# Kernel optimization log

Hardware: AMD Instinct MI355X
Metric: run time of the kernel (lower is better)

The kernel has to match this reference:

```python
import jax, jax.numpy as jnp
import numpy as np

H = 64       # hidden size hard-coded in the module
NH = 4       # n_heads
S = 500      # stock_num
D = 10       # num_day
T = 40       # num_text (news per day)
FP = 3       # price features
FT = 512     # text embedding dim


def gru_scan(x, Wih, Whh, bih, bhh):
    """Single-sequence GRU (torch gate convention). x: (T, F) -> hidden states (T, H)."""
    gi = x @ Wih + bih  # (T, 3H) precompute input gates outside the scan

    def step(h, g):
        gh = h @ Whh + bhh
        r = jax.nn.sigmoid(g[:H] + gh[:H])
        z = jax.nn.sigmoid(g[H:2 * H] + gh[H:2 * H])
        n = jnp.tanh(g[2 * H:] + r * gh[2 * H:])
        h_new = (1.0 - z) * n + z * h
        return h_new, h_new

    h0 = jnp.zeros((H,), x.dtype)
    _, hs = jax.lax.scan(step, h0, gi)
    return hs


def attn_pool(hs, W, v):
    """Additive attention pooling over time. hs: (T, H) -> (H,)."""
    scores = jnp.tanh(hs @ W) @ v          # (T,)
    alpha = jax.nn.softmax(scores)
    return alpha @ hs


def _gru_params(key, fin, scale=0.08):
    k1, k2, k3, k4 = jax.random.split(key, 4)
    return (jax.random.normal(k1, (S, fin, 3 * H)) * scale,
            jax.random.normal(k2, (S, H, 3 * H)) * scale,
            jax.random.normal(k3, (S, 3 * H)) * scale,
            jax.random.normal(k4, (S, 3 * H)) * scale)


def _attn_params(key, scale=0.08):
    k1, k2 = jax.random.split(key)
    return (jax.random.normal(k1, (S, H, H)) * scale,
            jax.random.normal(k2, (S, H)) * scale)


def setup_inputs() -> dict:
    key = jax.random.key(0)
    ks = jax.random.split(key, 20)
    inp = {}
    inp['text_input'] = jax.random.normal(ks[0], (S, D, T, FT), dtype=jnp.float32)
    inp['price_input'] = jax.random.normal(ks[1], (S, D, FP), dtype=jnp.float32)
    inp['label'] = jax.random.randint(ks[2], (S,), 0, 2)
    inp['adj'] = jnp.ones((S, S), dtype=jnp.float32)
    inp['train'] = 0
    # per-stock stacked parameters
    (inp['Wih_p'], inp['Whh_p'], inp['bih_p'], inp['bhh_p']) = _gru_params(ks[3], FP)
    (inp['Wa_p'], inp['va_p']) = _attn_params(ks[4])
    (inp['Wih_t'], inp['Whh_t'], inp['bih_t'], inp['bhh_t']) = _gru_params(ks[5], FT)
    (inp['Wa_t'], inp['va_t']) = _attn_params(ks[6])
    (inp['Wih_s'], inp['Whh_s'], inp['bih_s'], inp['bhh_s']) = _gru_params(ks[7], H)
    (inp['Wa_s'], inp['va_s']) = _attn_params(ks[8])
    inp['Wb'] = jax.random.normal(ks[9], (S, H, H, H)) * 0.05   # Bilinear weight (out,in1,in2)
    inp['bb'] = jax.random.normal(ks[10], (S, H)) * 0.05
    inp['Wbl'] = jax.random.normal(ks[11], (S, H, 2)) * 0.08
    inp['bbl'] = jax.random.normal(ks[12], (S, 2)) * 0.08
    # shared cross-stock self-attention projections and final fc
    inp['Wq'] = jax.random.normal(ks[13], (H, H)) * 0.08
    inp['bq'] = jax.random.normal(ks[14], (H,)) * 0.08
    inp['Wk'] = jax.random.normal(ks[15], (H, H)) * 0.08
    inp['bk'] = jax.random.normal(ks[16], (H,)) * 0.08
    inp['Wf'] = jax.random.normal(ks[17], (H, 2)) * 0.08
    inp['bf'] = jax.random.normal(ks[18], (2,)) * 0.08
    return inp


def _forward(text_input, price_input, label,
             Wih_p, Whh_p, bih_p, bhh_p, Wa_p, va_p,
             Wih_t, Whh_t, bih_t, bhh_t, Wa_t, va_t,
             Wih_s, Whh_s, bih_s, bhh_s, Wa_s, va_s,
             Wb, bb, Wbl, bbl, Wq, bq, Wk, bk, Wf, bf):
    # ---- per-stock price encoder: GRU over days + attention pooling ----
    def enc_price(x, a, b, c, d, W, v):
        return attn_pool(gru_scan(x, a, b, c, d), W, v)
    x_price = jax.vmap(enc_price)(price_input, Wih_p, Whh_p, bih_p, bhh_p, Wa_p, va_p)  # (S, H)

    # ---- per-stock, per-day text encoder ----
    def enc_text_stock(xdays, a, b, c, d, W, v):
        return jax.vmap(lambda x: attn_pool(gru_scan(x, a, b, c, d), W, v))(xdays)  # (D, H)
    news = jax.vmap(enc_text_stock)(text_input, Wih_t, Whh_t, bih_t, bhh_t, Wa_t, va_t)  # (S, D, H)

    # ---- per-stock sequence encoder over days ----
    text_vec = jax.vmap(enc_price)(news, Wih_s, Whh_s, bih_s, bhh_s, Wa_s, va_s)  # (S, H)

    # ---- bilinear fusion: tanh(Bilinear(text, price)) ----
    combined = jnp.tanh(jnp.einsum('si,skij,sj->sk', text_vec, Wb, x_price) + bb)  # (S, H)

    # ---- per-stock blending head ----
    out_1 = jnp.tanh(jnp.einsum('si,sik->sk', combined, Wbl) + bbl)  # (S, 2)

    # ---- cross-stock multi-head self-attention (q,k projected, v identity) ----
    dh = H // NH
    q = (combined @ Wq + bq).reshape(S, NH, dh)
    k = (combined @ Wk + bk).reshape(S, NH, dh)
    v = combined.reshape(S, NH, dh)
    scores = jnp.einsum('shd,thd->hst', q, k) / (dh ** 0.5)
    attn = jax.nn.softmax(scores, axis=-1)
    attn_out = jnp.einsum('hst,thd->shd', attn, v).reshape(S, H)

    x = jax.nn.elu(attn_out @ Wf + bf)  # (S, 2)
    output = jax.nn.softmax(x + out_1, axis=1)
    # faithful to the original: CrossEntropyLoss applied to already-softmaxed output
    logp = jax.nn.log_softmax(output, axis=1)
    loss = -jnp.mean(logp[jnp.arange(S), label])
    return loss, output


def reference(text_input, price_input, label, adj, train,
              Wih_p, Whh_p, bih_p, bhh_p, Wa_p, va_p,
              Wih_t, Whh_t, bih_t, bhh_t, Wa_t, va_t,
              Wih_s, Whh_s, bih_s, bhh_s, Wa_s, va_s,
              Wb, bb, Wbl, bbl, Wq, bq, Wk, bk, Wf, bf):
    return _forward(text_input, price_input, label,
                    Wih_p, Whh_p, bih_p, bhh_p, Wa_p, va_p,
                    Wih_t, Whh_t, bih_t, bhh_t, Wa_t, va_t,
                    Wih_s, Whh_s, bih_s, bhh_s, Wa_s, va_s,
                    Wb, bb, Wbl, bbl, Wq, bq, Wk, bk, Wf, bf)
```

## Files before the change

kernel.cpp:

```cpp
#include <hip/hip_runtime.h>

#define Sn 500
#define Dn 10
#define Tn 40
#define FPn 3
#define FTn 512
#define Hn 64
#define G3 192
#define NHn 4

typedef __attribute__((ext_vector_type(8))) short bf8_t;
typedef __attribute__((ext_vector_type(4))) float f4_t;

__device__ __forceinline__ unsigned short f2bf(float f) {
    union { float f; unsigned int u; } v; v.f = f;
    unsigned int r = v.u + 0x7fffu + ((v.u >> 16) & 1u);
    return (unsigned short)(r >> 16);
}
__device__ __forceinline__ float bflo(unsigned int u) {
    union { unsigned int u; float f; } v; v.u = u << 16; return v.f;
}
__device__ __forceinline__ float bfhi(unsigned int u) {
    union { unsigned int u; float f; } v; v.u = u & 0xffff0000u; return v.f;
}
__device__ __forceinline__ unsigned int cvtpk(float lo, float hi) {
    unsigned int r;
    asm("v_cvt_pk_bf16_f32 %0, %1, %2" : "=v"(r) : "v"(lo), "v"(hi));
    return r;
}
__device__ __forceinline__ float sigmoidf_(float x) { return 1.f / (1.f + __expf(-x)); }
__device__ __forceinline__ float tanhf_(float x) {
    x = fminf(15.f, fmaxf(-15.f, x));
    float e = __expf(2.f * x);
    return (e - 1.f) / (e + 1.f);
}
__device__ __forceinline__ float dot8(uint4 wv, f4_t hA, f4_t hB) {
    return bflo(wv.x) * hA[0] + bfhi(wv.x) * hA[1]
         + bflo(wv.y) * hA[2] + bfhi(wv.y) * hA[3]
         + bflo(wv.z) * hB[0] + bfhi(wv.z) * hB[1]
         + bflo(wv.w) * hB[2] + bfhi(wv.w) * hB[3];
}
union bfu { bf8_t v; unsigned int u[4]; };

__global__ __launch_bounds__(256, 3) void gi_gemm3(
    const float* __restrict__ text, const float* __restrict__ Wih,
    const float* __restrict__ bih, float* __restrict__ gi2)
{
    __shared__ __align__(16) unsigned char Asb[112 * 80];

    const int bid = blockIdx.x;
    const int swz = (bid & 7) * 250 + (bid >> 3);
    const int s = swz >> 2, q = swz & 3;
    const int tid = threadIdx.x, w = tid >> 6, l = tid & 63;
    const int lr = l & 15, lg = l >> 4;

    const float* Wihs = Wih + (size_t)s * FTn * G3;
    const float* xrow = text + ((size_t)s * 400 + q * 100) * FTn;

    if (tid < 240) ((unsigned int*)(Asb + 100 * 80))[tid] = 0u;

    f4_t acc[7][3];
    #pragma unroll
    for (int a = 0; a < 7; a++)
        #pragma unroll
        for (int b = 0; b < 3; b++) acc[a][b] = (f4_t){0.f, 0.f, 0.f, 0.f};

    f4_t pa0[2], pa1[2];
    auto loadT = [&](int kk) {
        #pragma unroll
        for (int u = 0; u < 2; ++u) {
            int tsk = tid + u * 256;
            if (tsk < 400) {
                int rw = tsk >> 2, ch = tsk & 3;
                const float* p = xrow + (size_t)rw * FTn + kk * 32 + ch * 8;
                pa0[u] = *(const f4_t*)p; pa1[u] = *(const f4_t*)(p + 4);
            }
        }
    };
    auto storeT = [&]() {
        #pragma unroll
        for (int u = 0; u < 2; ++u) {
            int tsk = tid + u * 256;
            if (tsk < 400) {
                int rw = tsk >> 2, ch = tsk & 3;
                uint4 uu = { cvtpk(pa0[u][0], pa0[u][1]), cvtpk(pa0[u][2], pa0[u][3]),
                             cvtpk(pa1[u][0], pa1[u][1]), cvtpk(pa1[u][2], pa1[u][3]) };
                *(uint4*)(Asb + rw * 80 + ch * 16) = uu;
            }
        }
    };

    loadT(0);
    for (int kk = 0; kk < 16; ++kk) {
        __syncthreads();
        storeT();
        __syncthreads();
        if (kk < 15) loadT(kk + 1);

        bfu bfr[3];
        #pragma unroll
        for (int nc = 0; nc < 3; ++nc) {
            const int col = w * 48 + nc * 16 + lr;
            const float* bp = Wihs + (size_t)(kk * 32 + lg * 8) * G3 + col;
            float b0 = bp[0], b1 = bp[G3], b2 = bp[2 * G3], b3 = bp[3 * G3];
            float b4 = bp[4 * G3], b5 = bp[5 * G3], b6 = bp[6 * G3], b7 = bp[7 * G3];
            bfr[nc].u[0] = cvtpk(b0, b1); bfr[nc].u[1] = cvtpk(b2, b3);
            bfr[nc].u[2] = cvtpk(b4, b5); bfr[nc].u[3] = cvtpk(b6, b7);
        }
        #pragma unroll
        for (int mt = 0; mt < 7; ++mt) {
            bf8_t af = *(const bf8_t*)(Asb + (mt * 16 + lr) * 80 + lg * 16);
            #pragma unroll
            for (int nc = 0; nc < 3; ++nc)
                acc[mt][nc] = __builtin_amdgcn_mfma_f32_16x16x32_bf16(af, bfr[nc].v, acc[mt][nc], 0, 0, 0);
        }
    }

    #pragma unroll
    for (int nc = 0; nc < 3; ++nc) {
        const int col = w * 48 + nc * 16 + lr;
        const int ntg = col >> 4;
        const float bv = bih[(size_t)s * G3 + col];
        #pragma unroll
        for (int mt = 0; mt < 7; ++mt) {
            #pragma unroll
            for (int rg = 0; rg < 4; ++rg) {
                int rl = mt * 16 + lg * 4 + rg;
                if (rl < 100) {
                    int row = q * 100 + rl;
                    int day = row / 40, t = row - day * 40;
                    size_t idx = (((size_t)s * 40 + t) * 48 + ntg * 4 + (day & 3)) * 64
                               + ((day >> 2) << 4) + lr;
                    gi2[idx] = acc[mt][nc][rg] + bv;
                }
            }
        }
    }
}

__global__ __launch_bounds__(64, 1) void gru_text_f(
    const float* __restrict__ gi2, const float* __restrict__ Whh,
    const float* __restrict__ bhh, const float* __restrict__ Wa,
    const float* __restrict__ va, float* __restrict__ news)
{
    __shared__ __align__(16) float hrow[16 * 68];
    __shared__ __align__(16) unsigned char waT[Hn * 128];

    const int s = blockIdx.x, l = threadIdx.x;
    const int lr = l & 15, lg = l >> 4;

    const float* Whhs = Whh + (size_t)s * Hn * G3;
    bfu bwhh[2][12];
    #pragma unroll
    for (int ks = 0; ks < 2; ++ks)
        #pragma unroll
        for (int nt = 0; nt < 12; ++nt) {
            const float* p = Whhs + (size_t)(ks * 32 + lg * 8) * G3 + nt * 16 + lr;
            float b0 = p[0], b1 = p[G3], b2 = p[2 * G3], b3 = p[3 * G3];
            float b4 = p[4 * G3], b5 = p[5 * G3], b6 = p[6 * G3], b7 = p[7 * G3];
            bwhh[ks][nt].u[0] = cvtpk(b0, b1); bwhh[ks][nt].u[1] = cvtpk(b2, b3);
            bwhh[ks][nt].u[2] = cvtpk(b4, b5); bwhh[ks][nt].u[3] = cvtpk(b6, b7);
        }
    float bhh_l[12];
    #pragma unroll
    for (int nt = 0; nt < 12; ++nt) bhh_l[nt] = bhh[(size_t)s * G3 + nt * 16 + lr];
    float va_l[4];
    #pragma unroll
    for (int nt = 0; nt < 4; ++nt) va_l[nt] = va[(size_t)s * Hn + nt * 16 + lr];

    {
        const float* Was = Wa + (size_t)s * Hn * Hn;
        for (int r = 0; r < 64; ++r) {
            int e = l + r * 64, i = e >> 6, k = e & 63;
            *(unsigned short*)(waT + k * 128 + ((2 * i) ^ ((k & 7) << 4))) = f2bf(Was[e]);
        }
        #pragma unroll
        for (int r = 0; r < 17; ++r) hrow[l + r * 64] = 0.f;
    }
    __builtin_amdgcn_wave_barrier();

    float val[48], valn[48];
    {
        const float* gb = gi2 + (size_t)s * 40 * 3072 + l;
        #pragma unroll
        for (int j = 0; j < 48; ++j) val[j] = gb[j * 64];
    }
    bf8_t a0f, a1f;
    {   bfu z0; z0.u[0] = 0; z0.u[1] = 0; z0.u[2] = 0; z0.u[3] = 0; a0f = z0.v; a1f = z0.v; }

    float h[4][4], accv[4][4], den[4], m[4];
    #pragma unroll
    for (int nt = 0; nt < 4; ++nt)
        #pragma unroll
        for (int rr = 0; rr < 4; ++rr) { h[nt][rr] = 0.f; accv[nt][rr] = 0.f; }
    #pragma unroll
    for (int rr = 0; rr < 4; ++rr) { den[rr] = 0.f; m[rr] = -1e30f; }

    for (int t = 0; t < Tn; ++t) {
        f4_t acc[12];
        #pragma unroll
        for (int nt = 0; nt < 12; ++nt)
            acc[nt] = (f4_t){bhh_l[nt], bhh_l[nt], bhh_l[nt], bhh_l[nt]};
        #pragma unroll
        for (int nt = 0; nt < 12; ++nt) {
            acc[nt] = __builtin_amdgcn_mfma_f32_16x16x32_bf16(a0f, bwhh[0][nt].v, acc[nt], 0, 0, 0);
            acc[nt] = __builtin_amdgcn_mfma_f32_16x16x32_bf16(a1f, bwhh[1][nt].v, acc[nt], 0, 0, 0);
        }
        {
            const int tn = (t < Tn - 1) ? t + 1 : t;
            const float* gb = gi2 + ((size_t)s * 40 + tn) * 3072 + l;
            #pragma unroll
            for (int j = 0; j < 48; ++j) valn[j] = gb[j * 64];
        }
        #pragma unroll
        for (int nt = 0; nt < 4; ++nt)
            #pragma unroll
            for (int rr = 0; rr < 4; ++rr) {
                float r = sigmoidf_(val[nt * 4 + rr] + acc[nt][rr]);
                float z = sigmoidf_(val[(nt + 4) * 4 + rr] + acc[nt + 4][rr]);
                float n = tanhf_(val[(nt + 8) * 4 + rr] + r * acc[nt + 8][rr]);
                h[nt][rr] = (1.f - z) * n + z * h[nt][rr];
            }
        __builtin_amdgcn_wave_barrier();
        #pragma unroll
        for (int rr = 0; rr < 4; ++rr) {
            int day = lg * 4 + rr;
            if (day < Dn) {
                #pragma unroll
                for (int nt = 0; nt < 4; ++nt) hrow[day * 68 + nt * 16 + lr] = h[nt][rr];
            }
        }
        __builtin_amdgcn_wave_barrier();
        {
            const float* hp = hrow + lr * 68 + lg * 8;
            f4_t x0 = *(const f4_t*)hp,        x1 = *(const f4_t*)(hp + 4);
            f4_t y0 = *(const f4_t*)(hp + 32), y1 = *(const f4_t*)(hp + 36);
            bfu t0, t1;
            t0.u[0] = cvtpk(x0[0], x0[1]); t0.u[1] = cvtpk(x0[2], x0[3]);
            t0.u[2] = cvtpk(x1[0], x1[1]); t0.u[3] = cvtpk(x1[2], x1[3]);
            t1.u[0] = cvtpk(y0[0], y0[1]); t1.u[1] = cvtpk(y0[2], y0[3]);
            t1.u[2] = cvtpk(y1[0], y1[1]); t1.u[3] = cvtpk(y1[2], y1[3]);
            a0f = t0.v; a1f = t1.v;
        }
        f4_t sc[4];
        #pragma unroll
        for (int nt = 0; nt < 4; ++nt) sc[nt] = (f4_t){0.f, 0.f, 0.f, 0.f};
        #pragma unroll
        for (int ks = 0; ks < 2; ++ks) {
            bf8_t av = ks ? a1f : a0f;
            #pragma unroll
            for (int nt = 0; nt < 4; ++nt) {
                bf8_t bwv = *(const bf8_t*)(waT + (nt * 16 + lr) * 128
                                            + ((ks * 64 + lg * 16) ^ ((lr & 7) << 4)));
                sc[nt] = __builtin_amdgcn_mfma_f32_16x16x32_bf16(av, bwv, sc[nt], 0, 0, 0);
            }
        }
        float pr[4];
        #pragma unroll
        for (int rr = 0; rr < 4; ++rr) {
            pr[rr] = tanhf_(sc[0][rr]) * va_l[0] + tanhf_(sc[1][rr]) * va_l[1]
                   + tanhf_(sc[2][rr]) * va_l[2] + tanhf_(sc[3][rr]) * va_l[3];
            pr[rr] += __shfl_xor(pr[rr], 1);
            pr[rr] += __shfl_xor(pr[rr], 2);
            pr[rr] += __shfl_xor(pr[rr], 4);
            pr[rr] += __shfl_xor(pr[rr], 8);
        }
        #pragma unroll
        for (int rr = 0; rr < 4; ++rr) {
            float mn = fmaxf(m[rr], pr[rr]);
            float s0 = __expf(m[rr] - mn);
            float p = __expf(pr[rr] - mn);
            den[rr] = den[rr] * s0 + p;
            #pragma unroll
            for (int nt = 0; nt < 4; ++nt)
                accv[nt][rr] = accv[nt][rr] * s0 + p * h[nt][rr];
            m[rr] = mn;
        }
        #pragma unroll
        for (int j = 0; j < 48; ++j) val[j] = valn[j];
    }
    #pragma unroll
    for (int rr = 0; rr < 4; ++rr) {
        int day = lg * 4 + rr;
        if (day < Dn) {
            float inv = 1.f / den[rr];
            #pragma unroll
            for (int nt = 0; nt < 4; ++nt)
                news[((size_t)s * Dn + day) * Hn + nt * 16 + lr] = accv[nt][rr] * inv;
        }
    }
}

__global__ __launch_bounds__(64, 1) void gru_small_f(
    const float* __restrict__ news,
    const float* __restrict__ Wih_s, const float* __restrict__ Whh_s,
    const float* __restrict__ bih_s, const float* __restrict__ bhh_s,
    const float* __restrict__ Wa_s, const float* __restrict__ va_s,
    const float* __restrict__ price, const float* __restrict__ Wih_p,
    const float* __restrict__ Whh_p, const float* __restrict__ bih_p,
    const float* __restrict__ bhh_p, const float* __restrict__ Wa_p,
    const float* __restrict__ va_p,
    float* __restrict__ tvec, float* __restrict__ xprice)
{
    __shared__ __align__(16) unsigned char sm[60928];
    unsigned char* whh2 = sm;
    unsigned char* wih2 = sm + 24576;
    unsigned char* wa2 = sm + 49152;
    float* newsL = (float*)(sm + 57600);
    float* hbuf  = (float*)(sm + 60320);
    float* priceL = (float*)(sm + 60608);

    const int s = blockIdx.x, l = threadIdx.x;

    {
        const float* W2 = Whh_s + (size_t)s * Hn * G3;
        const float* X2 = Wih_s + (size_t)s * Hn * G3;
        for (int r = 0; r < 192; ++r) {
            int e = l + r * 64, i = e / G3, j = e - i * G3;
            int off = j * 128 + ((2 * i) ^ ((j & 7) << 4));
            *(unsigned short*)(whh2 + off) = f2bf(W2[e]);
            *(unsigned short*)(wih2 + off) = f2bf(X2[e]);
        }
        const float* A2 = Wa_s + (size_t)s * Hn * Hn;
        for (int r = 0; r < 64; ++r) {
            int e = l + r * 64, i = e >> 6, k = e & 63;
            *(unsigned short*)(wa2 + k * 128 + ((2 * i) ^ ((k & 7) << 4))) = f2bf(A2[e]);
        }
        #pragma unroll
        for (int d = 0; d < Dn; ++d) newsL[d * 68 + l] = news[((size_t)s * Dn + d) * Hn + l];
        hbuf[l] = 0.f;
        if (l < 4) hbuf[64 + l] = 0.f;
    }
    __builtin_amdgcn_wave_barrier();
    {
        const float bi0 = bih_s[(size_t)s * G3 + l];
        const float bi1 = bih_s[(size_t)s * G3 + 64 + l];
        const float bi2 = bih_s[(size_t)s * G3 + 128 + l];
        const float bh0 = bhh_s[(size_t)s * G3 + l];
        const float bh1 = bhh_s[(size_t)s * G3 + 64 + l];
        const float bh2 = bhh_s[(size_t)s * G3 + 128 + l];
        const float vak = va_s[(size_t)s * Hn + l];
        const int swl = (l & 7) << 4;
        float h2 = 0.f, m2 = -1e30f, den2 = 0.f, av2 = 0.f;
        for (int t = 0; t < Dn; ++t) {
            float gh0 = bh0, gh1 = bh1, gh2 = bh2;
            float gg0 = bi0, gg1 = bi1, gg2 = bi2;
            #pragma unroll
            for (int ic = 0; ic < 8; ++ic) {
                const int off = (ic * 16) ^ swl;
                f4_t hA = *(const f4_t*)&hbuf[ic * 8];
                f4_t hB = *(const f4_t*)&hbuf[ic * 8 + 4];
                f4_t nA = *(const f4_t*)&newsL[t * 68 + ic * 8];
                f4_t nB = *(const f4_t*)&newsL[t * 68 + ic * 8 + 4];
                uint4 w0 = *(const uint4*)(whh2 + l * 128 + off);
                uint4 w1 = *(const uint4*)(whh2 + (l + 64) * 128 + off);
                uint4 w2 = *(const uint4*)(whh2 + (l + 128) * 128 + off);
                uint4 x0 = *(const uint4*)(wih2 + l * 128 + off);
                uint4 x1 = *(const uint4*)(wih2 + (l + 64) * 128 + off);
                uint4 x2 = *(const uint4*)(wih2 + (l + 128) * 128 + off);
                gh0 += dot8(w0, hA, hB); gh1 += dot8(w1, hA, hB); gh2 += dot8(w2, hA, hB);
                gg0 += dot8(x0, nA, nB); gg1 += dot8(x1, nA, nB); gg2 += dot8(x2, nA, nB);
            }
            float r = sigmoidf_(gg0 + gh0);
            float z = sigmoidf_(gg1 + gh1);
            float n = tanhf_(gg2 + r * gh2);
            h2 = (1.f - z) * n + z * h2;
            __builtin_amdgcn_wave_barrier();
            hbuf[l] = h2;
            __builtin_amdgcn_wave_barrier();
            float sk = 0.f;
            #pragma unroll
            for (int ic = 0; ic < 8; ++ic) {
                const int off = (ic * 16) ^ swl;
                uint4 wv = *(const uint4*)(wa2 + l * 128 + off);
                f4_t hA = *(const f4_t*)&hbuf[ic * 8];
                f4_t hB = *(const f4_t*)&hbuf[ic * 8 + 4];
                sk += dot8(wv, hA, hB);
            }
            float term = tanhf_(sk) * vak;
            #pragma unroll
            for (int off = 32; off; off >>= 1) term += __shfl_xor(term, off);
            float mn = fmaxf(m2, term);
            float s0 = __expf(m2 - mn);
            float p = __expf(term - mn);
            den2 = den2 * s0 + p;
            av2 = av2 * s0 + p * h2;
            m2 = mn;
        }
        tvec[(size_t)s * Hn + l] = av2 / den2;
    }
    __builtin_amdgcn_wave_barrier();

    {
        const float* W3 = Whh_p + (size_t)s * Hn * G3;
        for (int r = 0; r < 192; ++r) {
            int e = l + r * 64, i = e / G3, j = e - i * G3;
            *(unsigned short*)(whh2 + j * 128 + ((2 * i) ^ ((j & 7) << 4))) = f2bf(W3[e]);
        }
        const float* A3 = Wa_p + (size_t)s * Hn * Hn;
        for (int r = 0; r < 64; ++r) {
            int e = l + r * 64, i = e >> 6, k = e & 63;
            *(unsigned short*)(wa2 + k * 128 + ((2 * i) ^ ((k & 7) << 4))) = f2bf(A3[e]);
        }
        if (l < 30) priceL[l] = price[(size_t)s * 30 + l];
        hbuf[l] = 0.f;
        if (l < 4) hbuf[64 + l] = 0.f;
    }
    __builtin_amdgcn_wave_barrier();
    {
        float wp[3][3];
        #pragma unroll
        for (int i = 0; i < 3; ++i)
            #pragma unroll
            for (int g = 0; g < 3; ++g)
                wp[i][g] = Wih_p[(size_t)s * 3 * G3 + i * G3 + g * 64 + l];
        const float bi0 = bih_p[(size_t)s * G3 + l];
        const float bi1 = bih_p[(size_t)s * G3 + 64 + l];
        const float bi2 = bih_p[(size_t)s * G3 + 128 + l];
        const float bh0 = bhh_p[(size_t)s * G3 + l];
        const float bh1 = bhh_p[(size_t)s * G3 + 64 + l];
        const float bh2 = bhh_p[(size_t)s * G3 + 128 + l];
        const float vak = va_p[(size_t)s * Hn + l];
        const int swl = (l & 7) << 4;
        float h3 = 0.f, m3 = -1e30f, den3 = 0.f, av3 = 0.f;
        for (int t = 0; t < Dn; ++t) {
            float x0 = priceL[t * 3], x1 = priceL[t * 3 + 1], x2 = priceL[t * 3 + 2];
            float gg0 = bi0 + x0 * wp[0][0] + x1 * wp[1][0] + x2 * wp[2][0];
            float gg1 = bi1 + x0 * wp[0][1] + x1 * wp[1][1] + x2 * wp[2][1];
            float gg2 = bi2 + x0 * wp[0][2] + x1 * wp[1][2] + x2 * wp[2][2];
            float gh0 = bh0, gh1 = bh1, gh2 = bh2;
            #pragma unroll
            for (int ic = 0; ic < 8; ++ic) {
                const int off = (ic * 16) ^ swl;
                f4_t hA = *(const f4_t*)&hbuf[ic * 8];
                f4_t hB = *(const f4_t*)&hbuf[ic * 8 + 4];
                uint4 w0 = *(const uint4*)(whh2 + l * 128 + off);
                uint4 w1 = *(const uint4*)(whh2 + (l + 64) * 128 + off);
                uint4 w2 = *(const uint4*)(whh2 + (l + 128) * 128 + off);
                gh0 += dot8(w0, hA, hB); gh1 += dot8(w1, hA, hB); gh2 += dot8(w2, hA, hB);
            }
            float r = sigmoidf_(gg0 + gh0);
            float z = sigmoidf_(gg1 + gh1);
            float n = tanhf_(gg2 + r * gh2);
            h3 = (1.f - z) * n + z * h3;
            __builtin_amdgcn_wave_barrier();
            hbuf[l] = h3;
            __builtin_amdgcn_wave_barrier();
            float sk = 0.f;
            #pragma unroll
            for (int ic = 0; ic < 8; ++ic) {
                const int off = (ic * 16) ^ swl;
                uint4 wv = *(const uint4*)(wa2 + l * 128 + off);
                f4_t hA = *(const f4_t*)&hbuf[ic * 8];
                f4_t hB = *(const f4_t*)&hbuf[ic * 8 + 4];
                sk += dot8(wv, hA, hB);
            }
            float term = tanhf_(sk) * vak;
            #pragma unroll
            for (int off = 32; off; off >>= 1) term += __shfl_xor(term, off);
            float mn = fmaxf(m3, term);
            float s0 = __expf(m3 - mn);
            float p = __expf(term - mn);
            den3 = den3 * s0 + p;
            av3 = av3 * s0 + p * h3;
            m3 = mn;
        }
        xprice[(size_t)s * Hn + l] = av3 / den3;
    }
}

__global__ __launch_bounds__(256) void bilinear2(
    const float* __restrict__ Wb, const float* __restrict__ bb,
    const float* __restrict__ xprice, const float* __restrict__ tvec,
    float* __restrict__ combined)
{
    __shared__ __align__(16) float uT[Hn][32];
    __shared__ float tv[Hn];

    const int bid = blockIdx.x, s = bid >> 1, kh = bid & 1;
    const int tid = threadIdx.x;
    const int w = tid >> 6, l = tid & 63;
    if (tid < Hn) tv[tid] = tvec[s * Hn + tid];
    const int j4 = (l & 15) * 4;
    f4_t xq = *(const f4_t*)&xprice[s * Hn + j4];
    __syncthreads();

    const float* Wbs = Wb + (size_t)s * Hn * Hn * Hn;
    for (int g = 0; g < 128; ++g) {
        int P = kh * 2048 + w * 512 + g * 4 + (l >> 4);
        f4_t wv = *(const f4_t*)&Wbs[(size_t)P * Hn + j4];
        float dp = wv[0] * xq[0] + wv[1] * xq[1] + wv[2] * xq[2] + wv[3] * xq[3];
        dp += __shfl_xor(dp, 8);
        dp += __shfl_xor(dp, 4);
        dp += __shfl_xor(dp, 2);
        dp += __shfl_xor(dp, 1);
        if ((l & 15) == 0) { int k = P >> 6, i = P & 63; uT[i][k - kh * 32] = dp; }
    }
    __syncthreads();
    if (tid < 32) {
        const int k = kh * 32 + tid;
        float a = bb[s * Hn + k];
        for (int i = 0; i < Hn; i++) a += tv[i] * uT[i][tid];
        combined[s * Hn + k] = tanhf_(a);
    }
}

__global__ __launch_bounds__(64) void qk_proj(
    const float* __restrict__ combined, const float* __restrict__ Wq,
    const float* __restrict__ bq, const float* __restrict__ Wk,
    const float* __restrict__ bk, const float* __restrict__ Wbl,
    const float* __restrict__ bbl,
    float* __restrict__ qg, float* __restrict__ kg, float* __restrict__ out1)
{
    __shared__ float cl[Hn];
    const int s = blockIdx.x, l = threadIdx.x;
    cl[l] = combined[s * Hn + l];
    __syncthreads();
    float aq = bq[l], ak = bk[l];
    for (int i = 0; i < Hn; i++) {
        float ci = cl[i];
        aq += ci * Wq[i * Hn + l];
        ak += ci * Wk[i * Hn + l];
    }
    qg[s * Hn + l] = aq; kg[s * Hn + l] = ak;
    if (l < 2) {
        float a = bbl[s * 2 + l];
        for (int i = 0; i < Hn; i++) a += cl[i] * Wbl[(size_t)s * Hn * 2 + i * 2 + l];
        out1[s * 2 + l] = tanhf_(a);
    }
}

__global__ __launch_bounds__(256) void mhsa(
    const float* __restrict__ qg, const float* __restrict__ kg,
    const float* __restrict__ combined, const float* __restrict__ Wf,
    const float* __restrict__ bfp, const float* __restrict__ out1,
    float* __restrict__ dout)
{
    __shared__ __align__(16) float ql[Hn];
    __shared__ float sl[NHn][Sn];
    __shared__ float hsum[NHn];
    __shared__ float ao[Hn];
    __shared__ float red2[8];
    __shared__ float red3[4][Hn];

    const int sq = blockIdx.x, tid = threadIdx.x;
    if (tid < Hn) ql[tid] = qg[sq * Hn + tid];
    __syncthreads();

    for (int id = tid; id < Sn * NHn; id += 256) {
        int t = id >> 2, h = id & 3;
        const float* kp = &kg[t * Hn + h * 16];
        float a = 0.f;
        #pragma unroll
        for (int x = 0; x < 16; x += 4) {
            f4_t kv = *(const f4_t*)&kp[x];
            f4_t qv = *(const f4_t*)&ql[h * 16 + x];
            a += kv[0] * qv[0] + kv[1] * qv[1] + kv[2] * qv[2] + kv[3] * qv[3];
        }
        sl[h][t] = a * 0.25f;
    }
    __syncthreads();
    for (int h = 0; h < NHn; ++h) {
        float m = -1e30f;
        for (int t = tid; t < Sn; t += 256) m = fmaxf(m, sl[h][t]);
        for (int o = 32; o; o >>= 1) m = fmaxf(m, __shfl_xor(m, o));
        if ((tid & 63) == 0) red2[tid >> 6] = m;
        __syncthreads();
        m = fmaxf(fmaxf(red2[0], red2[1]), fmaxf(red2[2], red2[3]));
        float ps = 0.f;
        for (int t = tid; t < Sn; t += 256) { float p = __expf(sl[h][t] - m); sl[h][t] = p; ps += p; }
        for (int o = 32; o; o >>= 1) ps += __shfl_xor(ps, o);
        if ((tid & 63) == 0) red2[4 + (tid >> 6)] = ps;
        __syncthreads();
        if (tid == 0) hsum[h] = red2[4] + red2[5] + red2[6] + red2[7];
        __syncthreads();
    }
    {
        const int q = tid >> 6, j = tid & 63, h = j >> 4;
        float a = 0.f;
        for (int t = q * 125; t < q * 125 + 125; ++t) a += sl[h][t] * combined[t * Hn + j];
        red3[q][j] = a;
    }
    __syncthreads();
    if (tid < Hn)
        ao[tid] = (red3[0][tid] + red3[1][tid] + red3[2][tid] + red3[3][tid]) / hsum[tid >> 4];
    __syncthreads();
    if (tid == 0) {
        float l0 = bfp[0], l1 = bfp[1];
        for (int j = 0; j < Hn; j++) { float v = ao[j]; l0 += v * Wf[j * 2]; l1 += v * Wf[j * 2 + 1]; }
        l0 = l0 > 0.f ? l0 : __expf(l0) - 1.f;
        l1 = l1 > 0.f ? l1 : __expf(l1) - 1.f;
        l0 += out1[sq * 2]; l1 += out1[sq * 2 + 1];
        float m = fmaxf(l0, l1);
        float e0 = __expf(l0 - m), e1 = __expf(l1 - m);
        float inv = 1.f / (e0 + e1);
        dout[1 + sq * 2] = e0 * inv;
        dout[2 + sq * 2] = e1 * inv;
    }
}

__global__ __launch_bounds__(512) void loss_k(float* __restrict__ dout,
                                              const int* __restrict__ label)
{
    __shared__ float red[512];
    const int tid = threadIdx.x;
    float a = 0.f;
    if (tid < Sn) {
        float p0 = dout[1 + 2 * tid], p1 = dout[2 + 2 * tid];
        float m = fmaxf(p0, p1);
        float lse = m + __logf(__expf(p0 - m) + __expf(p1 - m));
        float pl = label[tid] ? p1 : p0;
        a = -(pl - lse);
    }
    red[tid] = a;
    __syncthreads();
    for (int o = 256; o; o >>= 1) {
        if (tid < o) red[tid] += red[tid + o];
        __syncthreads();
    }
    if (tid == 0) dout[0] = red[0] / (float)Sn;
}

extern "C" void kernel_launch(void* const* d_in, const int* in_sizes, int n_in,
                              void* d_out, int out_size, void* d_ws, size_t ws_size,
                              hipStream_t stream)
{
    const float* text  = (const float*)d_in[0];
    const float* price = (const float*)d_in[1];
    const int*   label = (const int*)  d_in[2];
    const float* Wih_p = (const float*)d_in[5];
    const float* Whh_p = (const float*)d_in[6];
    const float* bih_p = (const float*)d_in[7];
    const float* bhh_p = (const float*)d_in[8];
    const float* Wa_p  = (const float*)d_in[9];
    const float* va_p  = (const float*)d_in[10];
    const float* Wih_t = (const float*)d_in[11];
    const float* Whh_t = (const float*)d_in[12];
    const float* bih_t = (const float*)d_in[13];
    const float* bhh_t = (const float*)d_in[14];
    const float* Wa_t  = (const float*)d_in[15];
    const float* va_t  = (const float*)d_in[16];
    const float* Wih_s = (const float*)d_in[17];
    const float* Whh_s = (const float*)d_in[18];
    const float* bih_s = (const float*)d_in[19];
    const float* bhh_s = (const float*)d_in[20];
    const float* Wa_s  = (const float*)d_in[21];
    const float* va_s  = (const float*)d_in[22];
    const float* Wb    = (const float*)d_in[23];
    const float* bb    = (const float*)d_in[24];
    const float* Wbl   = (const float*)d_in[25];
    const float* bbl   = (const float*)d_in[26];
    const float* Wq    = (const float*)d_in[27];
    const float* bq    = (const float*)d_in[28];
    const float* Wk    = (const float*)d_in[29];
    const float* bk    = (const float*)d_in[30];
    const float* Wf    = (const float*)d_in[31];
    const float* bf_   = (const float*)d_in[32];

    float* ws = (float*)d_ws;
    float* news     = ws;
    float* xprice   = ws + 320000;
    float* tvec     = ws + 352000;
    float* combined = ws + 384000;
    float* qg       = ws + 416000;
    float* kg       = ws + 448000;
    float* out1     = ws + 480000;
    float* gi2      = ws + 481000;
    float* dout = (float*)d_out;

    gi_gemm3<<<Sn * 4, 256, 0, stream>>>(text, Wih_t, bih_t, gi2);
    gru_text_f<<<Sn, 64, 0, stream>>>(gi2, Whh_t, bhh_t, Wa_t, va_t, news);
    gru_small_f<<<Sn, 64, 0, stream>>>(news,
                                       Wih_s, Whh_s, bih_s, bhh_s, Wa_s, va_s,
                                       price, Wih_p, Whh_p, bih_p, bhh_p, Wa_p, va_p,
                                       tvec, xprice);
    bilinear2<<<Sn * 2, 256, 0, stream>>>(Wb, bb, xprice, tvec, combined);
    qk_proj<<<Sn, 64, 0, stream>>>(combined, Wq, bq, Wk, bk, Wbl, bbl, qg, kg, out1);
    mhsa<<<Sn, 256, 0, stream>>>(qg, kg, combined, Wf, bf_, out1, dout);
    loss_k<<<1, 512, 0, stream>>>(dout, label);
}
```

Baseline: 675.2 us.

## Load GEMM A-operand directly into registers and retile into 80-row blocks

The input-gate GEMM now skips the LDS staging buffer and its two barriers per k-step. Each lane loads its own MFMA A fragment straight from global memory and converts it to bf16 in registers, with the next k-slice prefetched. Work is split into 5 blocks of 80 rows per stock instead of 4 of 100, which removes the padded rows, and the XCD swizzle is adjusted for 2500 blocks. The gi2 layout changes to a plain (t, day, gate) order, so the GRU kernel's gather indices change to match. The costs are lower occupancy bounds, redundant A loads across the four waves (each wave loads the same A rows), and less coalesced gi2 reads in the recurrent kernel.

```diff
diff --git a/kernel.cpp b/kernel.cpp
--- a/kernel.cpp
+++ b/kernel.cpp
@@ -42,99 +42,82 @@
 }
 union bfu { bf8_t v; unsigned int u[4]; };
 
-__global__ __launch_bounds__(256, 3) void gi_gemm3(
+__global__ __launch_bounds__(256, 2) void gi_gemm4(
     const float* __restrict__ text, const float* __restrict__ Wih,
     const float* __restrict__ bih, float* __restrict__ gi2)
 {
-    __shared__ __align__(16) unsigned char Asb[112 * 80];
-
     const int bid = blockIdx.x;
-    const int swz = (bid & 7) * 250 + (bid >> 3);
-    const int s = swz >> 2, q = swz & 3;
+    const int xcd = bid & 7, ix = bid >> 3;
+    const int swz = (xcd < 4 ? xcd * 313 : 4 * 313 + (xcd - 4) * 312) + ix;
+    const int s = swz / 5, fi = swz % 5;
     const int tid = threadIdx.x, w = tid >> 6, l = tid & 63;
-    const int lr = l & 15, lg = l >> 4;
-
-    const float* Wihs = Wih + (size_t)s * FTn * G3;
-    const float* xrow = text + ((size_t)s * 400 + q * 100) * FTn;
-
-    if (tid < 240) ((unsigned int*)(Asb + 100 * 80))[tid] = 0u;
-
-    f4_t acc[7][3];
-    #pragma unroll
-    for (int a = 0; a < 7; a++)
+    const int lr = l & 15, kg = l >> 4;
+
+    const float* Wihs = Wih + (size_t)s * FTn * G3 + w * 48 + lr;
+    const float* xrow = text + ((size_t)s * 400 + fi * 80 + lr) * FTn + kg * 8;
+
+    f4_t acc[5][3];
+    #pragma unroll
+    for (int a = 0; a < 5; a++)
         #pragma unroll
         for (int b = 0; b < 3; b++) acc[a][b] = (f4_t){0.f, 0.f, 0.f, 0.f};
 
-    f4_t pa0[2], pa1[2];
-    auto loadT = [&](int kk) {
-        #pragma unroll
-        for (int u = 0; u < 2; ++u) {
-            int tsk = tid + u * 256;
-            if (tsk < 400) {
-                int rw = tsk >> 2, ch = tsk & 3;
-                const float* p = xrow + (size_t)rw * FTn + kk * 32 + ch * 8;
-                pa0[u] = *(const f4_t*)p; pa1[u] = *(const f4_t*)(p + 4);
-            }
-        }
-    };
-    auto storeT = [&]() {
-        #pragma unroll
-        for (int u = 0; u < 2; ++u) {
-            int tsk = tid + u * 256;
-            if (tsk < 400) {
-                int rw = tsk >> 2, ch = tsk & 3;
-                uint4 uu = { cvtpk(pa0[u][0], pa0[u][1]), cvtpk(pa0[u][2], pa0[u][3]),
-                             cvtpk(pa1[u][0], pa1[u][1]), cvtpk(pa1[u][2], pa1[u][3]) };
-                *(uint4*)(Asb + rw * 80 + ch * 16) = uu;
-            }
-        }
-    };
-
-    loadT(0);
+    f4_t an0[5], an1[5];
+    #pragma unroll
+    for (int mt = 0; mt < 5; ++mt) {
+        const float* p = xrow + (size_t)mt * 16 * FTn;
+        an0[mt] = *(const f4_t*)p; an1[mt] = *(const f4_t*)(p + 4);
+    }
+
     for (int kk = 0; kk < 16; ++kk) {
-        __syncthreads();
-        storeT();
-        __syncthreads();
-        if (kk < 15) loadT(kk + 1);
-
+        bfu af[5];
+        #pragma unroll
+        for (int mt = 0; mt < 5; ++mt) {
+            af[mt].u[0] = cvtpk(an0[mt][0], an0[mt][1]);
+            af[mt].u[1] = cvtpk(an0[mt][2], an0[mt][3]);
+            af[mt].u[2] = cvtpk(an1[mt][0], an1[mt][1]);
+            af[mt].u[3] = cvtpk(an1[mt][2], an1[mt][3]);
+        }
+        if (kk < 15) {
+            const float* px = xrow + (kk + 1) * 32;
+            #pragma unroll
+            for (int mt = 0; mt < 5; ++mt) {
+                const float* p = px + (size_t)mt * 16 * FTn;
+                an0[mt] = *(const f4_t*)p; an1[mt] = *(const f4_t*)(p + 4);
+            }
+        }
         bfu bfr[3];
+        const float* bp0 = Wihs + (size_t)(kk * 32 + kg * 8) * G3;
         #pragma unroll
         for (int nc = 0; nc < 3; ++nc) {
-            const int col = w * 48 + nc * 16 + lr;
-            const float* bp = Wihs + (size_t)(kk * 32 + lg * 8) * G3 + col;
+            const float* bp = bp0 + nc * 16;
             float b0 = bp[0], b1 = bp[G3], b2 = bp[2 * G3], b3 = bp[3 * G3];
             float b4 = bp[4 * G3], b5 = bp[5 * G3], b6 = bp[6 * G3], b7 = bp[7 * G3];
             bfr[nc].u[0] = cvtpk(b0, b1); bfr[nc].u[1] = cvtpk(b2, b3);
             bfr[nc].u[2] = cvtpk(b4, b5); bfr[nc].u[3] = cvtpk(b6, b7);
         }
         #pragma unroll
-        for (int mt = 0; mt < 7; ++mt) {
-            bf8_t af = *(const bf8_t*)(Asb + (mt * 16 + lr) * 80 + lg * 16);
+        for (int mt = 0; mt < 5; ++mt)
             #pragma unroll
             for (int nc = 0; nc < 3; ++nc)
-                acc[mt][nc] = __builtin_amdgcn_mfma_f32_16x16x32_bf16(af, bfr[nc].v, acc[mt][nc], 0, 0, 0);
-        }
-    }
-
+                acc[mt][nc] = __builtin_amdgcn_mfma_f32_16x16x32_bf16(af[mt].v, bfr[nc].v, acc[mt][nc], 0, 0, 0);
+    }
+
+    const float* bihs = bih + (size_t)s * G3 + w * 48 + lr;
     #pragma unroll
     for (int nc = 0; nc < 3; ++nc) {
         const int col = w * 48 + nc * 16 + lr;
-        const int ntg = col >> 4;
-        const float bv = bih[(size_t)s * G3 + col];
-        #pragma unroll
-        for (int mt = 0; mt < 7; ++mt) {
+        const float bv = bihs[nc * 16];
+        #pragma unroll
+        for (int mt = 0; mt < 5; ++mt)
             #pragma unroll
             for (int rg = 0; rg < 4; ++rg) {
-                int rl = mt * 16 + lg * 4 + rg;
-                if (rl < 100) {
-                    int row = q * 100 + rl;
-                    int day = row / 40, t = row - day * 40;
-                    size_t idx = (((size_t)s * 40 + t) * 48 + ntg * 4 + (day & 3)) * 64
-                               + ((day >> 2) << 4) + lr;
-                    gi2[idx] = acc[mt][nc][rg] + bv;
-                }
-            }
-        }
+                int r = mt * 16 + kg * 4 + rg;
+                int hi = (r >= 40);
+                int day = fi * 2 + hi;
+                int t = r - hi * 40;
+                gi2[((size_t)(s * 40 + t) * 10 + day) * 192 + col] = acc[mt][nc][rg] + bv;
+            }
     }
 }
 
@@ -179,12 +162,18 @@
     }
     __builtin_amdgcn_wave_barrier();
 
+    int dayoff[4];
+    #pragma unroll
+    for (int rr = 0; rr < 4; ++rr) {
+        int d = lg * 4 + rr; if (d > 9) d = 9;
+        dayoff[rr] = d * 192 + lr;
+    }
+    const float* gbase = gi2 + (size_t)s * 40 * 1920;
+
     float val[48], valn[48];
-    {
-        const float* gb = gi2 + (size_t)s * 40 * 3072 + l;
-        #pragma unroll
-        for (int j = 0; j < 48; ++j) val[j] = gb[j * 64];
-    }
+    #pragma unroll
+    for (int j = 0; j < 48; ++j) val[j] = gbase[dayoff[j & 3] + (j >> 2) * 16];
+
     bf8_t a0f, a1f;
     {   bfu z0; z0.u[0] = 0; z0.u[1] = 0; z0.u[2] = 0; z0.u[3] = 0; a0f = z0.v; a1f = z0.v; }
 
@@ -208,9 +197,9 @@
         }
         {
             const int tn = (t < Tn - 1) ? t + 1 : t;
-            const float* gb = gi2 + ((size_t)s * 40 + tn) * 3072 + l;
-            #pragma unroll
-            for (int j = 0; j < 48; ++j) valn[j] = gb[j * 64];
+            const float* gb = gbase + (size_t)tn * 1920;
+            #pragma unroll
+            for (int j = 0; j < 48; ++j) valn[j] = gb[dayoff[j & 3] + (j >> 2) * 16];
         }
         #pragma unroll
         for (int nt = 0; nt < 4; ++nt)
@@ -668,7 +657,7 @@
     float* gi2      = ws + 481000;
     float* dout = (float*)d_out;
 
-    gi_gemm3<<<Sn * 4, 256, 0, stream>>>(text, Wih_t, bih_t, gi2);
+    gi_gemm4<<<Sn * 5, 256, 0, stream>>>(text, Wih_t, bih_t, gi2);
     gru_text_f<<<Sn, 64, 0, stream>>>(gi2, Whh_t, bhh_t, Wa_t, va_t, news);
     gru_small_f<<<Sn, 64, 0, stream>>>(news,
                                        Wih_s, Whh_s, bih_s, bhh_s, Wa_s, va_s,
```

Result: no change. 663.1 us (-1.8%).
